# Performance work log

Measured on AMD Instinct MI355X. Metric: run time of the kernel, lower is better.

The kernel has to match this reference:

```python
import jax, jax.numpy as jnp
import numpy as np

B, L, D, H = 2, 4096, 1024, 4
DV = D // H
NP = 5
MIN_PROB = 0.01
CHUNK = 32
RIN = D + H * NP * 4 + H * (NP * (NP - 1)) // 2  # 1144
RH = 2 * RIN


def dwconv_causal(x, w):
    # x: (B, L, C); w: (C, K) depthwise causal FIR
    K = w.shape[-1]
    xp = jnp.pad(x, ((0, 0), (K - 1, 0), (0, 0))).transpose(0, 2, 1)  # (B,C,L+K-1)
    y = jax.lax.conv_general_dilated(
        xp, w[:, None, :], window_strides=(1,), padding='VALID',
        feature_group_count=w.shape[0],
        dimension_numbers=('NCH', 'OIH', 'NCH'))
    return y.transpose(0, 2, 1)  # (B,L,C)


def l2norm(x):
    return x * jax.lax.rsqrt(jnp.sum(x * x, -1, keepdims=True) + 1e-12)


def delta_rule_chunkwise(q, k, v, beta, chunk=CHUNK):
    # q,k: (b,h,L,dk)  v: (b,h,L,dv)  beta: (b,h,L); L divisible by chunk
    b, h, Lq, dk = q.shape
    dv = v.shape[-1]
    n = Lq // chunk
    q = l2norm(q); k = l2norm(k)
    v = v * beta[..., None]
    kb = k * beta[..., None]
    r = lambda x: x.reshape(b, h, n, chunk, -1)
    q, k, v, kb = r(q), r(k), r(v), r(kb)
    tri = jnp.triu(jnp.ones((chunk, chunk), bool), 0)
    attn = jnp.where(tri, 0.0, -(kb @ jnp.swapaxes(k, -1, -2)))
    for i in range(1, chunk):  # in-chunk triangular-inverse recurrence
        upd = jnp.einsum('...k,...ki->...i', attn[..., i, :], attn[..., :, :i])
        attn = attn.at[..., i, :i].add(upd)
    attn = attn + jnp.eye(chunk, dtype=attn.dtype)
    u = attn @ v
    w = attn @ kb
    strict = jnp.triu(jnp.ones((chunk, chunk), bool), 1)

    def step(S, inp):
        qi, ki, ui, wi = inp
        la = jnp.where(strict, 0.0, qi @ jnp.swapaxes(ki, -1, -2))
        u_i = ui - wi @ S
        o_i = qi @ S + la @ u_i
        return S + jnp.swapaxes(ki, -1, -2) @ u_i, o_i

    mv = lambda x: jnp.moveaxis(x, 2, 0)
    S0 = jnp.zeros((b, h, dk, dv), q.dtype)
    S, o = jax.lax.scan(step, S0, (mv(q), mv(k), mv(u), mv(w)))
    return jnp.moveaxis(o, 0, 2).reshape(b, h, Lq, dv), S


def setup_inputs() -> dict:
    key = jax.random.key(0)
    ks = jax.random.split(key, 20)
    f = lambda k, shape, s=0.02: jax.random.normal(k, shape, jnp.float32) * s
    # FIR filters: identity tap (last) + small noise, matching learned-from-delta init
    def fir(k, ksz):
        w = np.zeros((D, ksz), np.float32)
        w[:, -1] = 1.0
        return jnp.asarray(w) + f(k, (D, ksz), 0.02)
    b2 = np.zeros((H, NP), np.float32)
    b2[:, -1] = 0.5
    b2[:, -2] = 0.5
    return {
        'hidden_states': jax.random.normal(ks[0], (B, L, D), jnp.float32),
        'Wq': f(ks[1], (D, D)), 'Wk': f(ks[2], (D, D)), 'Wv': f(ks[3], (D, D)),
        'wq_conv': f(ks[4], (D, 4), 0.2), 'wk_conv': f(ks[5], (D, 4), 0.2),
        'wv_conv': f(ks[6], (D, 4), 0.2),
        'Wb': f(ks[7], (H, D)),
        'fir_s_w': fir(ks[8], 3), 'fir_m_w': fir(ks[9], 7),
        'fir_l_w': fir(ks[10], 25), 'fir_id_w': fir(ks[11], 1),
        'W1': f(ks[12], (RH, RIN)), 'b1': jnp.zeros((RH,), jnp.float32),
        'W2': f(ks[13], (H * NP, RH)), 'b2': jnp.asarray(b2.reshape(-1)),
        'norm_w': jnp.ones((DV,), jnp.float32),
        'Wo': f(ks[14], (D, D)),
    }


def reference(hidden_states, Wq, Wk, Wv, wq_conv, wk_conv, wv_conv, Wb,
              fir_s_w, fir_m_w, fir_l_w, fir_id_w, W1, b1, W2, b2, norm_w, Wo):
    silu = jax.nn.silu
    q = silu(dwconv_causal(hidden_states @ Wq.T, wq_conv))
    k = silu(dwconv_causal(hidden_states @ Wk.T, wk_conv))
    v = silu(dwconv_causal(hidden_states @ Wv.T, wv_conv))
    beta = jax.nn.sigmoid(hidden_states @ Wb.T)  # (B,L,H)
    q4 = q.reshape(B, L, H, -1).transpose(0, 2, 1, 3)
    k4 = k.reshape(B, L, H, -1).transpose(0, 2, 1, 3)
    v4 = v.reshape(B, L, H, -1).transpose(0, 2, 1, 3)
    delta_out, _ = delta_rule_chunkwise(q4, k4, v4, beta.transpose(0, 2, 1))
    delta_out = delta_out.transpose(0, 2, 1, 3)  # (B,L,H,DV)
    fir = lambda w: dwconv_causal(v, w).reshape(B, L, H, DV)
    branches = [fir(fir_s_w), fir(fir_m_w), fir(fir_l_w), delta_out, fir(fir_id_w)]
    feats = []
    for x in branches:
        sm = jax.nn.softmax(x, -1)
        feats += [x.mean(-1), jnp.var(x, -1, ddof=1), jnp.max(x, -1),
                  -(sm * jnp.log(sm + 1e-8)).sum(-1)]
    cross = []
    for i in range(NP):
        for j in range(i + 1, NP):
            xi, xj = branches[i], branches[j]
            den = jnp.sqrt(jnp.sum(xi * xi, -1)) * jnp.sqrt(jnp.sum(xj * xj, -1)) + 1e-8
            cross.append(jnp.sum(xi * xj, -1) / den)
    router_in = jnp.concatenate([hidden_states] + feats + cross, axis=-1)  # (B,L,RIN)
    hrt = jax.nn.gelu(router_in @ W1.T + b1, approximate=False)
    logits = (hrt @ W2.T + b2).reshape(B, L, H, NP)
    p = jax.nn.softmax(logits, -1)
    p = p * (1.0 - NP * MIN_PROB) + MIN_PROB  # probability floor
    out = jnp.einsum('blhp,pblhd->blhd', p, jnp.stack(branches))
    out = out * jax.lax.rsqrt(jnp.mean(out * out, -1, keepdims=True) + 1e-5) * norm_w
    return out.reshape(B, L, H * DV) @ Wo.T
```

## Files before the change

kernel.cpp:

```cpp
#include <hip/hip_runtime.h>
#include <stdint.h>

typedef unsigned short u16t;
typedef u16t us4 __attribute__((ext_vector_type(4)));
typedef u16t us8 __attribute__((ext_vector_type(8)));
typedef __bf16 bf8v __attribute__((ext_vector_type(8)));
typedef float f4 __attribute__((ext_vector_type(4)));

#define MFMA(a, b, c) __builtin_amdgcn_mfma_f32_16x16x32_bf16((a), (b), (c), 0, 0, 0)

__device__ __forceinline__ float bf2f(u16t u) {
  union { unsigned int i; float f; } c; c.i = ((unsigned int)u) << 16; return c.f;
}
__device__ __forceinline__ u16t f2bf(float f) {
  union { float f; unsigned int i; } c; c.f = f;
  return (u16t)((c.i + 0x7FFFu + ((c.i >> 16) & 1u)) >> 16);
}
__device__ __forceinline__ float wsum(float v) {
#pragma unroll
  for (int o = 32; o > 0; o >>= 1) v += __shfl_xor(v, o);
  return v;
}
__device__ __forceinline__ float wmax(float v) {
#pragma unroll
  for (int o = 32; o > 0; o >>= 1) v = fmaxf(v, __shfl_xor(v, o));
  return v;
}

template <bool AF32, bool BF32, bool CF32>
__device__ __forceinline__ void gemm_body(const void* __restrict__ Av,
    const void* __restrict__ Btv, void* __restrict__ Cv,
    int K, int lda, int ldb, int ldc, int m0, int n0) {
  __shared__ u16t As[128][40];
  __shared__ u16t Bs[128][40];
  const int tid = threadIdx.x;
  const int wv = tid >> 6, l = tid & 63;
  const int wr = wv >> 1, wc = wv & 1;
  const int lr = l & 15, kg8 = (l >> 4) * 8, rg4 = (l >> 4) * 4;
  const int row_s = tid >> 1, seg = (tid & 1) * 16;
  const f4 zf = {0.f, 0.f, 0.f, 0.f};
  f4 acc[4][4];
#pragma unroll
  for (int i = 0; i < 4; ++i)
#pragma unroll
    for (int j = 0; j < 4; ++j) acc[i][j] = zf;

  for (int kt = 0; kt < K; kt += 32) {
    us8 a0, a1, b0, b1;
    if (AF32) {
      const float* pa = (const float*)Av + (size_t)(m0 + row_s) * lda + seg + kt;
      f4 fa0 = *(const f4*)(pa), fa1 = *(const f4*)(pa + 4);
      f4 fa2 = *(const f4*)(pa + 8), fa3 = *(const f4*)(pa + 12);
#pragma unroll
      for (int e = 0; e < 4; ++e) {
        a0[e] = f2bf(fa0[e]); a0[e + 4] = f2bf(fa1[e]);
        a1[e] = f2bf(fa2[e]); a1[e + 4] = f2bf(fa3[e]);
      }
    } else {
      const u16t* pa = (const u16t*)Av + (size_t)(m0 + row_s) * lda + seg + kt;
      a0 = *(const us8*)(pa); a1 = *(const us8*)(pa + 8);
    }
    if (BF32) {
      const float* pb = (const float*)Btv + (size_t)(n0 + row_s) * ldb + seg + kt;
      f4 fb0 = *(const f4*)(pb), fb1 = *(const f4*)(pb + 4);
      f4 fb2 = *(const f4*)(pb + 8), fb3 = *(const f4*)(pb + 12);
#pragma unroll
      for (int e = 0; e < 4; ++e) {
        b0[e] = f2bf(fb0[e]); b0[e + 4] = f2bf(fb1[e]);
        b1[e] = f2bf(fb2[e]); b1[e + 4] = f2bf(fb3[e]);
      }
    } else {
      const u16t* pb = (const u16t*)Btv + (size_t)(n0 + row_s) * ldb + seg + kt;
      b0 = *(const us8*)(pb); b1 = *(const us8*)(pb + 8);
    }
    *(us8*)&As[row_s][seg] = a0;
    *(us8*)&As[row_s][seg + 8] = a1;
    *(us8*)&Bs[row_s][seg] = b0;
    *(us8*)&Bs[row_s][seg + 8] = b1;
    __syncthreads();
    bf8v af[4], bg[4];
#pragma unroll
    for (int f = 0; f < 4; ++f) af[f] = *(const bf8v*)&As[wr * 64 + f * 16 + lr][kg8];
#pragma unroll
    for (int f = 0; f < 4; ++f) bg[f] = *(const bf8v*)&Bs[wc * 64 + f * 16 + lr][kg8];
#pragma unroll
    for (int i = 0; i < 4; ++i)
#pragma unroll
      for (int j = 0; j < 4; ++j) acc[i][j] = MFMA(af[i], bg[j], acc[i][j]);
    __syncthreads();
  }
#pragma unroll
  for (int i = 0; i < 4; ++i) {
    const int rb = m0 + wr * 64 + i * 16 + rg4;
#pragma unroll
    for (int j = 0; j < 4; ++j) {
      const int cb = n0 + wc * 64 + j * 16 + lr;
#pragma unroll
      for (int r = 0; r < 4; ++r) {
        if (CF32)
          ((float*)Cv)[(size_t)(rb + r) * ldc + cb] = acc[i][j][r];
        else
          ((u16t*)Cv)[(size_t)(rb + r) * ldc + cb] = f2bf(acc[i][j][r]);
      }
    }
  }
}

template <bool AF32, bool BF32, bool CF32>
__global__ __launch_bounds__(256) void gemm_bt(const void* __restrict__ Av,
    const void* __restrict__ Btv, void* __restrict__ Cv,
    int K, int lda, int ldb, int ldc) {
  gemm_body<AF32, BF32, CF32>(Av, Btv, Cv, K, lda, ldb, ldc,
                              blockIdx.y * 128, blockIdx.x * 128);
}

__global__ __launch_bounds__(256) void gemm_qkv3(const float* __restrict__ A,
    const float* __restrict__ B0, const float* __restrict__ B1,
    const float* __restrict__ B2, u16t* __restrict__ C0, u16t* __restrict__ C1,
    u16t* __restrict__ C2v) {
  const int z = blockIdx.z;
  const float* Bt = (z == 0) ? B0 : ((z == 1) ? B1 : B2);
  u16t* C = (z == 0) ? C0 : ((z == 1) ? C1 : C2v);
  gemm_body<true, true, false>(A, Bt, C, 1024, 1024, 1024, 1024,
                               blockIdx.y * 128, blockIdx.x * 128);
}

__global__ __launch_bounds__(256) void conv4_silu(
    const u16t* __restrict__ qlin, const u16t* __restrict__ klin, const u16t* __restrict__ vlin,
    const float* __restrict__ wq, const float* __restrict__ wk, const float* __restrict__ wvv,
    u16t* __restrict__ qc, u16t* __restrict__ kc, u16t* __restrict__ vc) {
  const int tid = threadIdx.x;
  const int l0 = blockIdx.x * 64;
  const int b = blockIdx.y >> 2, cb = blockIdx.y & 3;
  const int z = blockIdx.z;
  const u16t* in_ = (z == 0) ? qlin : ((z == 1) ? klin : vlin);
  const float* w_ = (z == 0) ? wq : ((z == 1) ? wk : wvv);
  u16t* out_ = (z == 0) ? qc : ((z == 1) ? kc : vc);
  const int c = cb * 256 + tid;
  __shared__ u16t sm[67][256];
  for (int i = 0; i < 67; ++i) {
    int ls = l0 - 3 + i;
    sm[i][tid] = (ls >= 0) ? in_[((size_t)b * 4096 + ls) * 1024 + c] : (u16t)0;
  }
  __syncthreads();
  f4 w4 = *(const f4*)&w_[c * 4];
  for (int ll = 0; ll < 64; ++ll) {
    float y = bf2f(sm[ll][tid]) * w4[0] + bf2f(sm[ll + 1][tid]) * w4[1] +
              bf2f(sm[ll + 2][tid]) * w4[2] + bf2f(sm[ll + 3][tid]) * w4[3];
    y = y / (1.f + expf(-y));
    out_[((size_t)b * 4096 + l0 + ll) * 1024 + c] = f2bf(y);
  }
}

__global__ __launch_bounds__(256) void beta_kernel(const float* __restrict__ hid,
    const float* __restrict__ Wb, float* __restrict__ beta) {
  const int m = blockIdx.x, tid = threadIdx.x;
  const int h = tid >> 6, l = tid & 63;
  float acc = 0.f;
#pragma unroll
  for (int it = 0; it < 4; ++it) {
    int kk = l * 4 + it * 256;
    f4 hv = *(const f4*)&hid[(size_t)m * 1024 + kk];
    f4 wv4 = *(const f4*)&Wb[(size_t)h * 1024 + kk];
#pragma unroll
    for (int e = 0; e < 4; ++e) acc += hv[e] * wv4[e];
  }
  acc = wsum(acc);
  if (l == 0) beta[m * 4 + h] = 1.f / (1.f + expf(-acc));
}

__global__ __launch_bounds__(256) void prep_kernel(u16t* __restrict__ qc, u16t* __restrict__ kc,
    const u16t* __restrict__ vc, const float* __restrict__ beta,
    u16t* __restrict__ kbeta, u16t* __restrict__ vbeta) {
  const int m = blockIdx.x, tid = threadIdx.x;
  const int h = tid >> 6, l = tid & 63;
  const size_t base = (size_t)m * 1024 + h * 256 + l * 4;
  const float bet = beta[m * 4 + h];
  us4 q4 = *(const us4*)&qc[base];
  float qf[4]; float ss = 0.f;
#pragma unroll
  for (int e = 0; e < 4; ++e) { qf[e] = bf2f(q4[e]); ss += qf[e] * qf[e]; }
  float qsc = rsqrtf(wsum(ss) + 1e-12f);
  us4 qo;
#pragma unroll
  for (int e = 0; e < 4; ++e) qo[e] = f2bf(qf[e] * qsc);
  *(us4*)&qc[base] = qo;
  us4 k4 = *(const us4*)&kc[base];
  float kf[4]; ss = 0.f;
#pragma unroll
  for (int e = 0; e < 4; ++e) { kf[e] = bf2f(k4[e]); ss += kf[e] * kf[e]; }
  float ksc = rsqrtf(wsum(ss) + 1e-12f);
  us4 ko, kbo;
#pragma unroll
  for (int e = 0; e < 4; ++e) {
    float kn = kf[e] * ksc;
    ko[e] = f2bf(kn);
    kbo[e] = f2bf(kn * bet);
  }
  *(us4*)&kc[base] = ko;
  *(us4*)&kbeta[base] = kbo;
  us4 v4 = *(const us4*)&vc[base];
  us4 vo;
#pragma unroll
  for (int e = 0; e < 4; ++e) vo[e] = f2bf(bf2f(v4[e]) * bet);
  *(us4*)&vbeta[base] = vo;
}

__global__ __launch_bounds__(256) void chunk_uw(const u16t* __restrict__ kn,
    const u16t* __restrict__ kbeta, const u16t* __restrict__ vbeta,
    u16t* __restrict__ ug, u16t* __restrict__ wg) {
  const int tid = threadIdx.x;
  const int bh = blockIdx.x >> 7, ci = blockIdx.x & 127;
  const int b = bh >> 2, h = bh & 3;
  const int l0 = ci * 32;
  __shared__ u16t kns[32][264], kbs[32][264], vbs[32][264];
  __shared__ float attn_s[32][33];
  const int sr = tid >> 5, sd8 = (tid & 31) * 8;
  const size_t rowbase = (size_t)b * 4096 * 1024 + (size_t)h * 256;
#pragma unroll
  for (int i = 0; i < 4; ++i) {
    int r = i * 8 + sr;
    size_t g = rowbase + (size_t)(l0 + r) * 1024 + sd8;
    *(us8*)&kns[r][sd8] = *(const us8*)&kn[g];
    *(us8*)&kbs[r][sd8] = *(const us8*)&kbeta[g];
    *(us8*)&vbs[r][sd8] = *(const us8*)&vbeta[g];
  }
  __syncthreads();
  {
    const int i = tid >> 3, j4 = (tid & 7) * 4;
    float d0 = 0.f, d1 = 0.f, d2 = 0.f, d3 = 0.f;
    for (int d8 = 0; d8 < 256; d8 += 8) {
      us8 kb8 = *(const us8*)&kbs[i][d8];
      us8 n0v = *(const us8*)&kns[j4][d8];
      us8 n1v = *(const us8*)&kns[j4 + 1][d8];
      us8 n2v = *(const us8*)&kns[j4 + 2][d8];
      us8 n3v = *(const us8*)&kns[j4 + 3][d8];
#pragma unroll
      for (int e = 0; e < 8; ++e) {
        float kv = bf2f(kb8[e]);
        d0 += kv * bf2f(n0v[e]); d1 += kv * bf2f(n1v[e]);
        d2 += kv * bf2f(n2v[e]); d3 += kv * bf2f(n3v[e]);
      }
    }
    attn_s[i][j4]     = (j4     < i) ? -d0 : 0.f;
    attn_s[i][j4 + 1] = (j4 + 1 < i) ? -d1 : 0.f;
    attn_s[i][j4 + 2] = (j4 + 2 < i) ? -d2 : 0.f;
    attn_s[i][j4 + 3] = (j4 + 3 < i) ? -d3 : 0.f;
  }
  __syncthreads();
  if (tid < 32) {
    const int j = tid;
    for (int i = 1; i < 32; ++i) {
      float aij = attn_s[i][j];
      float upd = 0.f;
#pragma unroll 1
      for (int k = 1; k < 31; ++k) {
        float aik = __shfl(aij, k);
        float akj = (k > j && k < i) ? attn_s[k][j] : 0.f;
        upd += aik * akj;
      }
      if (j < i) attn_s[i][j] = aij + upd;
    }
    attn_s[j][j] = 1.f;
  }
  __syncthreads();
  {
    const int r = tid >> 3, cg = (tid & 7) * 32;
    float ua[32], wa[32];
#pragma unroll
    for (int e = 0; e < 32; ++e) { ua[e] = 0.f; wa[e] = 0.f; }
    for (int j = 0; j < 32; ++j) {
      float a = attn_s[r][j];
#pragma unroll
      for (int e0 = 0; e0 < 32; e0 += 8) {
        us8 v8 = *(const us8*)&vbs[j][cg + e0];
        us8 k8 = *(const us8*)&kbs[j][cg + e0];
#pragma unroll
        for (int e = 0; e < 8; ++e) {
          ua[e0 + e] += a * bf2f(v8[e]);
          wa[e0 + e] += a * bf2f(k8[e]);
        }
      }
    }
    const size_t ob = ((size_t)bh * 4096 + l0 + r) * 256 + cg;
#pragma unroll
    for (int e0 = 0; e0 < 32; e0 += 8) {
      us8 pu, pw;
#pragma unroll
      for (int e = 0; e < 8; ++e) { pu[e] = f2bf(ua[e0 + e]); pw[e] = f2bf(wa[e0 + e]); }
      *(us8*)&ug[ob + e0] = pu;
      *(us8*)&wg[ob + e0] = pw;
    }
  }
}

__global__ __launch_bounds__(256, 1) void delta_scan(const u16t* __restrict__ qn,
    const u16t* __restrict__ kn, const u16t* __restrict__ ug, const u16t* __restrict__ wg,
    u16t* __restrict__ dout) {
  const int blk = blockIdx.x;
  const int bh = blk >> 2, vbidx = blk & 3;
  const int b = bh >> 2, h = bh & 3;
  const int c0 = vbidx * 64;
  const int tid = threadIdx.x;
  const int wv = tid >> 6, l = tid & 63;
  const int lr = l & 15, kg8 = (l >> 4) * 8, rg4 = (l >> 4) * 4;

  __shared__ u16t qs[32][264], ks2[32][264], wss[32][264];
  __shared__ u16t kts[256][40];
  __shared__ u16t sbf[64][264];
  __shared__ u16t las[32][40];
  __shared__ u16t uts[64][40];

  {
    u16t* sp = &sbf[0][0];
    for (int i = tid; i < 64 * 264; i += 256) sp[i] = 0;
  }
  const f4 zf = {0.f, 0.f, 0.f, 0.f};
  f4 sacc[16];
#pragma unroll
  for (int d = 0; d < 16; ++d) sacc[d] = zf;
  __syncthreads();

  const u16t* qb = qn + (size_t)b * 4096 * 1024 + (size_t)h * 256;
  const u16t* knb = kn + (size_t)b * 4096 * 1024 + (size_t)h * 256;
  const u16t* ub = ug + (size_t)bh * 4096 * 256;
  const u16t* wb = wg + (size_t)bh * 4096 * 256;
  const int sr = tid >> 5, sd8 = (tid & 31) * 8;

  us8 pq[4], pk[4], pw[4];
  us4 pu0, pu1;
  {
#pragma unroll
    for (int i = 0; i < 4; ++i) {
      const int r = i * 8 + sr;
      pq[i] = *(const us8*)(qb + (size_t)r * 1024 + sd8);
      pk[i] = *(const us8*)(knb + (size_t)r * 1024 + sd8);
      pw[i] = *(const us8*)(wb + (size_t)r * 256 + sd8);
    }
    pu0 = *(const us4*)(ub + (size_t)lr * 256 + c0 + wv * 16 + rg4);
    pu1 = *(const us4*)(ub + (size_t)(16 + lr) * 256 + c0 + wv * 16 + rg4);
  }

  for (int ci = 0; ci < 128; ++ci) {
    const int l0 = ci * 32;
#pragma unroll
    for (int i = 0; i < 4; ++i) {
      const int r = i * 8 + sr;
      *(us8*)&qs[r][sd8] = pq[i];
      *(us8*)&ks2[r][sd8] = pk[i];
      *(us8*)&wss[r][sd8] = pw[i];
    }
    const us4 u0 = pu0, u1 = pu1;
    __syncthreads();
    if (ci < 127) {
      const int l1 = l0 + 32;
#pragma unroll
      for (int i = 0; i < 4; ++i) {
        const int r = i * 8 + sr;
        pq[i] = *(const us8*)(qb + (size_t)(l1 + r) * 1024 + sd8);
        pk[i] = *(const us8*)(knb + (size_t)(l1 + r) * 1024 + sd8);
        pw[i] = *(const us8*)(wb + (size_t)(l1 + r) * 256 + sd8);
      }
      pu0 = *(const us4*)(ub + (size_t)(l1 + lr) * 256 + c0 + wv * 16 + rg4);
      pu1 = *(const us4*)(ub + (size_t)(l1 + 16 + lr) * 256 + c0 + wv * 16 + rg4);
    }
    {
      const int dk = tid;
      const int swz = ((dk >> 3) & 3) << 3;
#pragma unroll
      for (int r = 0; r < 32; r += 2) {
        unsigned int lo = ks2[r][dk], hi = ks2[r + 1][dk];
        *(unsigned int*)&kts[dk][r ^ swz] = lo | (hi << 16);
      }
    }
    {
      const int rq = wv >> 1, rk = wv & 1;
      f4 t4 = zf;
#pragma unroll
      for (int ks = 0; ks < 8; ++ks) {
        bf8v a = *(const bf8v*)&qs[rq * 16 + lr][ks * 32 + kg8];
        bf8v bb = *(const bf8v*)&ks2[rk * 16 + lr][ks * 32 + kg8];
        t4 = MFMA(a, bb, t4);
      }
      const int colj = rk * 16 + lr;
#pragma unroll
      for (int rr = 0; rr < 4; ++rr) {
        const int rowr = rq * 16 + rg4 + rr;
        las[rowr][colj] = (colj <= rowr) ? f2bf(t4[rr]) : (u16t)0;
      }
    }
    f4 o0 = zf, o1 = zf;
    {
      f4 m0 = zf, m1 = zf;
#pragma unroll
      for (int ks = 0; ks < 8; ++ks) {
        bf8v a = *(const bf8v*)&sbf[wv * 16 + lr][ks * 32 + kg8];
        bf8v wb0 = *(const bf8v*)&wss[lr][ks * 32 + kg8];
        bf8v wb1 = *(const bf8v*)&wss[16 + lr][ks * 32 + kg8];
        bf8v qb0 = *(const bf8v*)&qs[lr][ks * 32 + kg8];
        bf8v qb1 = *(const bf8v*)&qs[16 + lr][ks * 32 + kg8];
        m0 = MFMA(a, wb0, m0);
        m1 = MFMA(a, wb1, m1);
        o0 = MFMA(a, qb0, o0);
        o1 = MFMA(a, qb1, o1);
      }
#pragma unroll
      for (int rt = 0; rt < 2; ++rt) {
        f4 mm = rt ? m1 : m0;
        const us4 uu = rt ? u1 : u0;
        const int r = rt * 16 + lr;
#pragma unroll
        for (int rr = 0; rr < 4; ++rr)
          uts[wv * 16 + rg4 + rr][r] = f2bf(bf2f(uu[rr]) - mm[rr]);
      }
    }
    __syncthreads();
    {
      bf8v a2 = *(const bf8v*)&uts[wv * 16 + lr][kg8];
      {
        bf8v lb0 = *(const bf8v*)&las[lr][kg8];
        bf8v lb1 = *(const bf8v*)&las[16 + lr][kg8];
        o0 = MFMA(a2, lb0, o0);
        o1 = MFMA(a2, lb1, o1);
      }
#pragma unroll
      for (int rt = 0; rt < 2; ++rt) {
        f4 oo = rt ? o1 : o0;
        const int r = rt * 16 + lr;
        us4 st;
#pragma unroll
        for (int rr = 0; rr < 4; ++rr) st[rr] = f2bf(oo[rr]);
        *(us4*)(dout + ((size_t)(b * 4096 + l0 + r) * 4 + h) * 256 + c0 + wv * 16 + rg4) = st;
      }
#pragma unroll
      for (int d = 0; d < 16; ++d) {
        const int swzd = ((2 * d + (lr >> 3)) & 3) << 3;
        bf8v bb = *(const bf8v*)&kts[d * 16 + lr][kg8 ^ swzd];
        sacc[d] = MFMA(a2, bb, sacc[d]);
      }
#pragma unroll
      for (int d = 0; d < 16; ++d) {
#pragma unroll
        for (int rr = 0; rr < 4; ++rr)
          sbf[wv * 16 + rg4 + rr][d * 16 + lr] = f2bf(sacc[d][rr]);
      }
    }
    __syncthreads();
  }
}

__global__ __launch_bounds__(256) void fir_kernel(const u16t* __restrict__ vc,
    const float* __restrict__ w3g, const float* __restrict__ w7g,
    const float* __restrict__ w25g, const float* __restrict__ w1g,
    u16t* __restrict__ fs, u16t* __restrict__ fm, u16t* __restrict__ fl,
    u16t* __restrict__ fid) {
  const int tid = threadIdx.x;
  const int l0 = blockIdx.x * 64;
  const int b = blockIdx.y >> 2, cb = blockIdx.y & 3;
  const int c = cb * 256 + tid;
  __shared__ u16t sm[88][256];
  for (int i = 0; i < 88; ++i) {
    int ls = l0 - 24 + i;
    sm[i][tid] = (ls >= 0) ? vc[((size_t)b * 4096 + ls) * 1024 + c] : (u16t)0;
  }
  __syncthreads();
  float w3[3], w7[7], w25[25], w1_;
#pragma unroll
  for (int j = 0; j < 3; ++j) w3[j] = w3g[c * 3 + j];
#pragma unroll
  for (int j = 0; j < 7; ++j) w7[j] = w7g[c * 7 + j];
#pragma unroll
  for (int j = 0; j < 25; ++j) w25[j] = w25g[c * 25 + j];
  w1_ = w1g[c];
  for (int ll = 0; ll < 64; ++ll) {
    float x[25];
#pragma unroll
    for (int j = 0; j < 25; ++j) x[j] = bf2f(sm[ll + j][tid]);
    float ys = x[22] * w3[0] + x[23] * w3[1] + x[24] * w3[2];
    float ym = 0.f;
#pragma unroll
    for (int j = 0; j < 7; ++j) ym += x[18 + j] * w7[j];
    float yl = 0.f;
#pragma unroll
    for (int j = 0; j < 25; ++j) yl += x[j] * w25[j];
    float yi = x[24] * w1_;
    const size_t o = ((size_t)b * 4096 + l0 + ll) * 1024 + c;
    fs[o] = f2bf(ys); fm[o] = f2bf(ym); fl[o] = f2bf(yl); fid[o] = f2bf(yi);
  }
}

__global__ __launch_bounds__(256) void features_kernel(const float* __restrict__ hid,
    const u16t* __restrict__ p0, const u16t* __restrict__ p1, const u16t* __restrict__ p2,
    const u16t* __restrict__ p3, const u16t* __restrict__ p4, u16t* __restrict__ router) {
  const int m = blockIdx.x, tid = threadIdx.x;
  const int h = tid >> 6, l = tid & 63;
  const size_t base = (size_t)m * 1024 + h * 256 + l * 4;
  const u16t* bp[5] = {p0, p1, p2, p3, p4};
  float x[5][4];
#pragma unroll
  for (int br = 0; br < 5; ++br) {
    us4 v = *(const us4*)&bp[br][base];
#pragma unroll
    for (int e = 0; e < 4; ++e) x[br][e] = bf2f(v[e]);
  }
  float s1[5], s2[5], mx[5];
#pragma unroll
  for (int br = 0; br < 5; ++br) {
    float a = 0.f, bq = 0.f, m_ = -1e30f;
#pragma unroll
    for (int e = 0; e < 4; ++e) {
      a += x[br][e]; bq += x[br][e] * x[br][e]; m_ = fmaxf(m_, x[br][e]);
    }
    s1[br] = wsum(a); s2[br] = wsum(bq); mx[br] = wmax(m_);
  }
  float ent[5];
#pragma unroll
  for (int br = 0; br < 5; ++br) {
    float e_ = 0.f;
#pragma unroll
    for (int e = 0; e < 4; ++e) e_ += expf(x[br][e] - mx[br]);
    float es = wsum(e_);
    float hn = 0.f;
#pragma unroll
    for (int e = 0; e < 4; ++e) {
      float pv = expf(x[br][e] - mx[br]) / es;
      hn += pv * logf(pv + 1e-8f);
    }
    ent[br] = -wsum(hn);
  }
  float dt[10];
  {
    int pi = 0;
#pragma unroll
    for (int i = 0; i < 5; ++i)
#pragma unroll
      for (int j = i + 1; j < 5; ++j) {
        float d = 0.f;
#pragma unroll
        for (int e = 0; e < 4; ++e) d += x[i][e] * x[j][e];
        dt[pi] = wsum(d);
        ++pi;
      }
  }
  if (l == 0) {
    u16t* rp = router + (size_t)m * 1152 + 1024;
#pragma unroll
    for (int br = 0; br < 5; ++br) {
      float mean = s1[br] * (1.f / 256.f);
      float var = (s2[br] - s1[br] * s1[br] * (1.f / 256.f)) * (1.f / 255.f);
      rp[br * 16 + 0 + h] = f2bf(mean);
      rp[br * 16 + 4 + h] = f2bf(var);
      rp[br * 16 + 8 + h] = f2bf(mx[br]);
      rp[br * 16 + 12 + h] = f2bf(ent[br]);
    }
    int pi = 0;
#pragma unroll
    for (int i = 0; i < 5; ++i)
#pragma unroll
      for (int j = i + 1; j < 5; ++j) {
        float den = sqrtf(s2[i]) * sqrtf(s2[j]) + 1e-8f;
        rp[80 + pi * 4 + h] = f2bf(dt[pi] / den);
        ++pi;
      }
  }
  {
    f4 hv = *(const f4*)&hid[(size_t)m * 1024 + tid * 4];
    us4 hv4;
#pragma unroll
    for (int e = 0; e < 4; ++e) hv4[e] = f2bf(hv[e]);
    *(us4*)&router[(size_t)m * 1152 + tid * 4] = hv4;
  }
  if (tid < 8) router[(size_t)m * 1152 + 1144 + tid] = 0;
}

__global__ __launch_bounds__(256) void gelu_bias(u16t* __restrict__ hrt,
    const float* __restrict__ b1) {
  const size_t idx = ((size_t)blockIdx.x * 256 + threadIdx.x) * 4;
  const int col = (int)(idx % 2304);
  us4 v = *(const us4*)&hrt[idx];
  us4 o;
#pragma unroll
  for (int e = 0; e < 4; ++e) {
    int cc = col + e;
    float xx = bf2f(v[e]) + ((cc < 2288) ? b1[cc] : 0.f);
    float g = 0.5f * xx * (1.f + erff(xx * 0.70710678118f));
    o[e] = f2bf(g);
  }
  *(us4*)&hrt[idx] = o;
}

__global__ __launch_bounds__(256) void w2_softmax(const u16t* __restrict__ hrt,
    const float* __restrict__ W2, const float* __restrict__ b2, float* __restrict__ pout) {
  const int m = blockIdx.x, tid = threadIdx.x;
  const int h = tid >> 6, l = tid & 63;
  float acc[5];
#pragma unroll
  for (int n = 0; n < 5; ++n) acc[n] = 0.f;
  for (int kk = l * 4; kk < 2288; kk += 256) {
    us4 hv = *(const us4*)&hrt[(size_t)m * 2304 + kk];
    float hf[4];
#pragma unroll
    for (int e = 0; e < 4; ++e) hf[e] = bf2f(hv[e]);
#pragma unroll
    for (int n = 0; n < 5; ++n) {
      f4 wv4 = *(const f4*)&W2[(size_t)(h * 5 + n) * 2288 + kk];
#pragma unroll
      for (int e = 0; e < 4; ++e) acc[n] += hf[e] * wv4[e];
    }
  }
#pragma unroll
  for (int n = 0; n < 5; ++n) acc[n] = wsum(acc[n]);
  if (l == 0) {
    float lg[5];
#pragma unroll
    for (int n = 0; n < 5; ++n) lg[n] = acc[n] + b2[h * 5 + n];
    float mxv = lg[0];
#pragma unroll
    for (int n = 1; n < 5; ++n) mxv = fmaxf(mxv, lg[n]);
    float es = 0.f, ev[5];
#pragma unroll
    for (int n = 0; n < 5; ++n) { ev[n] = expf(lg[n] - mxv); es += ev[n]; }
#pragma unroll
    for (int n = 0; n < 5; ++n)
      pout[(size_t)m * 20 + h * 5 + n] = (ev[n] / es) * 0.95f + 0.01f;
  }
}

__global__ __launch_bounds__(256) void mix_kernel(const u16t* __restrict__ p0,
    const u16t* __restrict__ p1, const u16t* __restrict__ p2, const u16t* __restrict__ p3,
    const u16t* __restrict__ p4, const float* __restrict__ pbuf,
    const float* __restrict__ normw, u16t* __restrict__ mixed) {
  const int m = blockIdx.x, tid = threadIdx.x;
  const int h = tid >> 6, l = tid & 63;
  const size_t base = (size_t)m * 1024 + h * 256 + l * 4;
  const u16t* bp[5] = {p0, p1, p2, p3, p4};
  float p5[5];
#pragma unroll
  for (int n = 0; n < 5; ++n) p5[n] = pbuf[(size_t)m * 20 + h * 5 + n];
  float o[4] = {0.f, 0.f, 0.f, 0.f};
#pragma unroll
  for (int br = 0; br < 5; ++br) {
    us4 v = *(const us4*)&bp[br][base];
#pragma unroll
    for (int e = 0; e < 4; ++e) o[e] += p5[br] * bf2f(v[e]);
  }
  float ss = 0.f;
#pragma unroll
  for (int e = 0; e < 4; ++e) ss += o[e] * o[e];
  ss = wsum(ss);
  float sc = rsqrtf(ss * (1.f / 256.f) + 1e-5f);
  f4 nw = *(const f4*)&normw[l * 4];
  us4 ov;
#pragma unroll
  for (int e = 0; e < 4; ++e) ov[e] = f2bf(o[e] * sc * nw[e]);
  *(us4*)&mixed[base] = ov;
}

__global__ __launch_bounds__(256) void pad_w1(const float* __restrict__ W1,
    u16t* __restrict__ W1p) {
  size_t idx = (size_t)blockIdx.x * 256 + threadIdx.x;
  if (idx >= (size_t)2304 * 1152) return;
  int n = (int)(idx / 1152), k = (int)(idx % 1152);
  W1p[idx] = (n < 2288 && k < 1144) ? f2bf(W1[(size_t)n * 1144 + k]) : (u16t)0;
}

extern "C" void kernel_launch(void* const* d_in, const int* in_sizes, int n_in,
                              void* d_out, int out_size, void* d_ws, size_t ws_size,
                              hipStream_t stream) {
  (void)in_sizes; (void)n_in; (void)out_size; (void)ws_size;
  const float* hid = (const float*)d_in[0];
  const float* Wq = (const float*)d_in[1];
  const float* Wk = (const float*)d_in[2];
  const float* Wv = (const float*)d_in[3];
  const float* wqc = (const float*)d_in[4];
  const float* wkc = (const float*)d_in[5];
  const float* wvc = (const float*)d_in[6];
  const float* Wb = (const float*)d_in[7];
  const float* fsw = (const float*)d_in[8];
  const float* fmw = (const float*)d_in[9];
  const float* flw = (const float*)d_in[10];
  const float* fiw = (const float*)d_in[11];
  const float* W1 = (const float*)d_in[12];
  const float* b1 = (const float*)d_in[13];
  const float* W2 = (const float*)d_in[14];
  const float* b2 = (const float*)d_in[15];
  const float* nwt = (const float*)d_in[16];
  const float* Wo = (const float*)d_in[17];
  float* out = (float*)d_out;

  char* wsp = (char*)d_ws;
  const size_t S = (size_t)2 * 4096 * 1024 * 2;
  u16t* ql = (u16t*)(wsp + 0 * S);
  u16t* kl = (u16t*)(wsp + 1 * S);
  u16t* vl = (u16t*)(wsp + 2 * S);
  u16t* qc = (u16t*)(wsp + 3 * S);
  u16t* kc = (u16t*)(wsp + 4 * S);
  u16t* vc = (u16t*)(wsp + 5 * S);
  u16t* ubuf = (u16t*)(wsp + 6 * S);
  u16t* wbuf = (u16t*)(wsp + 7 * S);
  char* p = wsp + 8 * S;
  u16t* router = (u16t*)p; p += (size_t)8192 * 1152 * 2;
  u16t* hrt = (u16t*)p;    p += (size_t)8192 * 2304 * 2;
  u16t* w1p = (u16t*)p;    p += (size_t)2304 * 1152 * 2;
  float* pbuf = (float*)p; p += (size_t)8192 * 20 * 4;
  float* beta = (float*)p; p += (size_t)8192 * 4 * 4;
  u16t* kbeta = ql;
  u16t* vbeta = kl;
  u16t* dlt = kl;
  u16t* f_s = vl;
  u16t* f_m = qc;
  u16t* f_l = kc;
  u16t* f_i = ubuf;
  u16t* mixed = wbuf;

  dim3 blk(256);
  gemm_qkv3<<<dim3(8, 64, 3), blk, 0, stream>>>(hid, Wq, Wk, Wv, ql, kl, vl);
  conv4_silu<<<dim3(64, 8, 3), blk, 0, stream>>>(ql, kl, vl, wqc, wkc, wvc, qc, kc, vc);
  beta_kernel<<<dim3(8192), blk, 0, stream>>>(hid, Wb, beta);
  prep_kernel<<<dim3(8192), blk, 0, stream>>>(qc, kc, vc, beta, kbeta, vbeta);
  chunk_uw<<<dim3(1024), blk, 0, stream>>>(kc, kbeta, vbeta, ubuf, wbuf);
  delta_scan<<<dim3(32), blk, 0, stream>>>(qc, kc, ubuf, wbuf, dlt);
  fir_kernel<<<dim3(64, 8), blk, 0, stream>>>(vc, fsw, fmw, flw, fiw, f_s, f_m, f_l, f_i);
  features_kernel<<<dim3(8192), blk, 0, stream>>>(hid, f_s, f_m, f_l, dlt, f_i, router);
  pad_w1<<<dim3(10368), blk, 0, stream>>>(W1, w1p);
  gemm_bt<false, false, false><<<dim3(18, 64), blk, 0, stream>>>(router, w1p, hrt, 1152, 1152, 1152, 2304);
  gelu_bias<<<dim3(18432), blk, 0, stream>>>(hrt, b1);
  w2_softmax<<<dim3(8192), blk, 0, stream>>>(hrt, W2, b2, pbuf);
  mix_kernel<<<dim3(8192), blk, 0, stream>>>(f_s, f_m, f_l, dlt, f_i, pbuf, nwt, mixed);
  gemm_bt<false, true, true><<<dim3(8, 64), blk, 0, stream>>>(mixed, Wo, out, 1024, 1024, 1024, 1024);
}
```

Measured before the change: 1.136 ms.

## Split delta scan into more, smaller blocks; slide FIR windows in registers

The sequential delta-rule scan now launches 64 blocks of 128 threads, each owning a 32-column slice of the value dimension, instead of 32 blocks of 256 threads owning 64 columns. Work on the serial chunk loop is spread over more CUs, but every block now loads the shared q/k/w tiles and recomputes the QK^T and transpose work for its slice, which duplicates that work and traffic. The causal conv and FIR kernels also keep a sliding window of inputs in registers rather than re-reading every tap from LDS on each step.

```diff
diff --git a/kernel.cpp b/kernel.cpp
--- a/kernel.cpp
+++ b/kernel.cpp
@@ -144,11 +144,13 @@
   }
   __syncthreads();
   f4 w4 = *(const f4*)&w_[c * 4];
+  float x0 = bf2f(sm[0][tid]), x1 = bf2f(sm[1][tid]), x2 = bf2f(sm[2][tid]);
   for (int ll = 0; ll < 64; ++ll) {
-    float y = bf2f(sm[ll][tid]) * w4[0] + bf2f(sm[ll + 1][tid]) * w4[1] +
-              bf2f(sm[ll + 2][tid]) * w4[2] + bf2f(sm[ll + 3][tid]) * w4[3];
+    float x3 = bf2f(sm[ll + 3][tid]);
+    float y = x0 * w4[0] + x1 * w4[1] + x2 * w4[2] + x3 * w4[3];
     y = y / (1.f + expf(-y));
     out_[((size_t)b * 4096 + l0 + ll) * 1024 + c] = f2bf(y);
+    x0 = x1; x1 = x2; x2 = x3;
   }
 }
 
@@ -294,26 +296,26 @@
   }
 }
 
-__global__ __launch_bounds__(256, 1) void delta_scan(const u16t* __restrict__ qn,
+__global__ __launch_bounds__(128, 1) void delta_scan(const u16t* __restrict__ qn,
     const u16t* __restrict__ kn, const u16t* __restrict__ ug, const u16t* __restrict__ wg,
     u16t* __restrict__ dout) {
   const int blk = blockIdx.x;
-  const int bh = blk >> 2, vbidx = blk & 3;
+  const int bh = blk >> 3, slice = blk & 7;
   const int b = bh >> 2, h = bh & 3;
-  const int c0 = vbidx * 64;
+  const int c0 = slice * 32;
   const int tid = threadIdx.x;
   const int wv = tid >> 6, l = tid & 63;
   const int lr = l & 15, kg8 = (l >> 4) * 8, rg4 = (l >> 4) * 4;
 
   __shared__ u16t qs[32][264], ks2[32][264], wss[32][264];
   __shared__ u16t kts[256][40];
-  __shared__ u16t sbf[64][264];
+  __shared__ u16t sbf[32][264];
   __shared__ u16t las[32][40];
-  __shared__ u16t uts[64][40];
+  __shared__ u16t uts[32][40];
 
   {
     u16t* sp = &sbf[0][0];
-    for (int i = tid; i < 64 * 264; i += 256) sp[i] = 0;
+    for (int i = tid; i < 32 * 264; i += 128) sp[i] = 0;
   }
   const f4 zf = {0.f, 0.f, 0.f, 0.f};
   f4 sacc[16];
@@ -327,12 +329,12 @@
   const u16t* wb = wg + (size_t)bh * 4096 * 256;
   const int sr = tid >> 5, sd8 = (tid & 31) * 8;
 
-  us8 pq[4], pk[4], pw[4];
+  us8 pq[8], pk[8], pw[8];
   us4 pu0, pu1;
   {
 #pragma unroll
-    for (int i = 0; i < 4; ++i) {
-      const int r = i * 8 + sr;
+    for (int i = 0; i < 8; ++i) {
+      const int r = i * 4 + sr;
       pq[i] = *(const us8*)(qb + (size_t)r * 1024 + sd8);
       pk[i] = *(const us8*)(knb + (size_t)r * 1024 + sd8);
       pw[i] = *(const us8*)(wb + (size_t)r * 256 + sd8);
@@ -344,8 +346,8 @@
   for (int ci = 0; ci < 128; ++ci) {
     const int l0 = ci * 32;
 #pragma unroll
-    for (int i = 0; i < 4; ++i) {
-      const int r = i * 8 + sr;
+    for (int i = 0; i < 8; ++i) {
+      const int r = i * 4 + sr;
       *(us8*)&qs[r][sd8] = pq[i];
       *(us8*)&ks2[r][sd8] = pk[i];
       *(us8*)&wss[r][sd8] = pw[i];
@@ -355,8 +357,8 @@
     if (ci < 127) {
       const int l1 = l0 + 32;
 #pragma unroll
-      for (int i = 0; i < 4; ++i) {
-        const int r = i * 8 + sr;
+      for (int i = 0; i < 8; ++i) {
+        const int r = i * 4 + sr;
         pq[i] = *(const us8*)(qb + (size_t)(l1 + r) * 1024 + sd8);
         pk[i] = *(const us8*)(knb + (size_t)(l1 + r) * 1024 + sd8);
         pw[i] = *(const us8*)(wb + (size_t)(l1 + r) * 256 + sd8);
@@ -365,28 +367,34 @@
       pu1 = *(const us4*)(ub + (size_t)(l1 + 16 + lr) * 256 + c0 + wv * 16 + rg4);
     }
     {
-      const int dk = tid;
-      const int swz = ((dk >> 3) & 3) << 3;
-#pragma unroll
-      for (int r = 0; r < 32; r += 2) {
-        unsigned int lo = ks2[r][dk], hi = ks2[r + 1][dk];
-        *(unsigned int*)&kts[dk][r ^ swz] = lo | (hi << 16);
+      for (int dk = tid; dk < 256; dk += 128) {
+        const int swz = ((dk >> 3) & 3) << 3;
+#pragma unroll
+        for (int r = 0; r < 32; r += 2) {
+          unsigned int lo = ks2[r][dk], hi = ks2[r + 1][dk];
+          *(unsigned int*)&kts[dk][r ^ swz] = lo | (hi << 16);
+        }
       }
     }
     {
-      const int rq = wv >> 1, rk = wv & 1;
-      f4 t4 = zf;
+      f4 t0 = zf, t1 = zf;
 #pragma unroll
       for (int ks = 0; ks < 8; ++ks) {
-        bf8v a = *(const bf8v*)&qs[rq * 16 + lr][ks * 32 + kg8];
-        bf8v bb = *(const bf8v*)&ks2[rk * 16 + lr][ks * 32 + kg8];
-        t4 = MFMA(a, bb, t4);
-      }
-      const int colj = rk * 16 + lr;
-#pragma unroll
-      for (int rr = 0; rr < 4; ++rr) {
-        const int rowr = rq * 16 + rg4 + rr;
-        las[rowr][colj] = (colj <= rowr) ? f2bf(t4[rr]) : (u16t)0;
+        bf8v a = *(const bf8v*)&qs[wv * 16 + lr][ks * 32 + kg8];
+        bf8v bb0 = *(const bf8v*)&ks2[lr][ks * 32 + kg8];
+        bf8v bb1 = *(const bf8v*)&ks2[16 + lr][ks * 32 + kg8];
+        t0 = MFMA(a, bb0, t0);
+        t1 = MFMA(a, bb1, t1);
+      }
+#pragma unroll
+      for (int rk = 0; rk < 2; ++rk) {
+        const f4 tt = rk ? t1 : t0;
+        const int colj = rk * 16 + lr;
+#pragma unroll
+        for (int rr = 0; rr < 4; ++rr) {
+          const int rowr = wv * 16 + rg4 + rr;
+          las[rowr][colj] = (colj <= rowr) ? f2bf(tt[rr]) : (u16t)0;
+        }
       }
     }
     f4 o0 = zf, o1 = zf;
@@ -472,10 +480,10 @@
 #pragma unroll
   for (int j = 0; j < 25; ++j) w25[j] = w25g[c * 25 + j];
   w1_ = w1g[c];
+  float x[25];
+#pragma unroll
+  for (int j = 0; j < 25; ++j) x[j] = bf2f(sm[j][tid]);
   for (int ll = 0; ll < 64; ++ll) {
-    float x[25];
-#pragma unroll
-    for (int j = 0; j < 25; ++j) x[j] = bf2f(sm[ll + j][tid]);
     float ys = x[22] * w3[0] + x[23] * w3[1] + x[24] * w3[2];
     float ym = 0.f;
 #pragma unroll
@@ -486,6 +494,11 @@
     float yi = x[24] * w1_;
     const size_t o = ((size_t)b * 4096 + l0 + ll) * 1024 + c;
     fs[o] = f2bf(ys); fm[o] = f2bf(ym); fl[o] = f2bf(yl); fid[o] = f2bf(yi);
+    if (ll < 63) {
+#pragma unroll
+      for (int j = 0; j < 24; ++j) x[j] = x[j + 1];
+      x[24] = bf2f(sm[ll + 25][tid]);
+    }
   }
 }
 
@@ -719,7 +732,7 @@
   beta_kernel<<<dim3(8192), blk, 0, stream>>>(hid, Wb, beta);
   prep_kernel<<<dim3(8192), blk, 0, stream>>>(qc, kc, vc, beta, kbeta, vbeta);
   chunk_uw<<<dim3(1024), blk, 0, stream>>>(kc, kbeta, vbeta, ubuf, wbuf);
-  delta_scan<<<dim3(32), blk, 0, stream>>>(qc, kc, ubuf, wbuf, dlt);
+  delta_scan<<<dim3(64), dim3(128), 0, stream>>>(qc, kc, ubuf, wbuf, dlt);
   fir_kernel<<<dim3(64, 8), blk, 0, stream>>>(vc, fsw, fmw, flw, fiw, f_s, f_m, f_l, f_i);
   features_kernel<<<dim3(8192), blk, 0, stream>>>(hid, f_s, f_m, f_l, dlt, f_i, router);
   pad_w1<<<dim3(10368), blk, 0, stream>>>(W1, w1p);
```

Result: no change. 1.157 ms (+1.9%).
